# Performance work log

Hardware: AMD Instinct MI355X
Metric: run time of the kernel (lower is better)

The kernel has to match this reference:

```python
import jax, jax.numpy as jnp
import numpy as np

B, N, D, W, IMG = 16384, 20, 64, 64, 2048
NUM_USERS, NUM_ITEMS, NUM_INGRE = 100000, 201000, 33001


def setup_inputs() -> dict:
    key = jax.random.key(0)
    ks = jax.random.split(key, 24)
    s = lambda *sh: 1.0 / np.sqrt(sh[0])
    inp = {
        'user_input': jax.random.randint(ks[0], (B,), 0, NUM_USERS),
        'item_input': jax.random.randint(ks[1], (B,), 0, NUM_ITEMS),
        'ingre_input': jax.random.randint(ks[2], (B, N), 0, NUM_INGRE),
        'image_input': jax.random.normal(ks[3], (B, IMG), dtype=jnp.float32),
        'ingre_num': jax.random.randint(ks[4], (B,), 1, N + 1),
        'user_emb': jax.random.normal(ks[5], (NUM_USERS, D), dtype=jnp.float32) * 0.01,
        'item_emb': jax.random.normal(ks[6], (NUM_ITEMS, D), dtype=jnp.float32) * 0.01,
        'ingre_emb': jax.random.normal(ks[7], (NUM_INGRE, D), dtype=jnp.float32) * 0.01,
        'W_image_w': jax.random.normal(ks[8], (IMG, D), dtype=jnp.float32) * s(IMG),
        'W_image_b': jnp.zeros((D,), jnp.float32),
        'b_image': jnp.zeros((1, D), jnp.float32),
        'W_concat_w': jax.random.normal(ks[9], (3 * D, D), dtype=jnp.float32) * s(3 * D),
        'W_concat_b': jnp.zeros((D,), jnp.float32),
        'b_concat': jnp.zeros((1, D), jnp.float32),
        'h_w': jax.random.normal(ks[10], (D, 1), dtype=jnp.float32) * s(D),
        'h_b': jnp.zeros((1,), jnp.float32),
        'W_att_ingre_w': jax.random.normal(ks[11], (3 * D, W), dtype=jnp.float32) * s(3 * D),
        'W_att_ingre_b': jnp.zeros((W,), jnp.float32),
        'b_att_ingre': jnp.zeros((1, W), jnp.float32),
        'v': jnp.ones((W, 1), jnp.float32),
        'W_att_com_w': jax.random.normal(ks[12], (2 * D, W), dtype=jnp.float32) * s(2 * D),
        'W_att_com_b': jnp.zeros((W,), jnp.float32),
        'b_att_com': jnp.zeros((1, W), jnp.float32),
        'v_c': jnp.ones((W, 1), jnp.float32),
    }
    return inp


def reference(user_input, item_input, ingre_input, image_input, ingre_num,
              user_emb, item_emb, ingre_emb,
              W_image_w, W_image_b, b_image,
              W_concat_w, W_concat_b, b_concat, h_w, h_b,
              W_att_ingre_w, W_att_ingre_b, b_att_ingre, v,
              W_att_com_w, W_att_com_b, b_att_com, v_c):
    b = user_input.shape[0]
    ue = user_emb[user_input]                       # [B, D]
    ie = item_emb[item_input]                       # [B, D]
    qe = ingre_emb[ingre_input]                     # [B, N, D]
    img = image_input @ W_image_w + W_image_b + b_image  # [B, D]

    # ---- ingredient-level attention ----
    n = qe.shape[1]
    tile_p = jnp.broadcast_to(ue[:, None, :], (b, n, ue.shape[-1]))
    tile_i = jnp.broadcast_to(img[:, None, :], (b, n, img.shape[-1]))
    concat_v = jnp.concatenate([qe, tile_p, tile_i], axis=2)     # [B, N, 3D]
    mlp = jnp.tanh(concat_v @ W_att_ingre_w + W_att_ingre_b + b_att_ingre[0])  # [B, N, W]
    A_ = (mlp @ v)[..., 0]                                        # [B, N]
    mask = (jnp.arange(n)[None, :] < ingre_num[:, None]).astype(A_.dtype)
    A_ = A_ * mask + (1.0 - mask) * (-1e12)
    A = jax.nn.softmax(A_, axis=1)[..., None]                     # [B, N, 1]
    ingre_att = jnp.sum(A * qe, axis=1)                           # [B, D]

    # ---- component-level attention (faithful to original cat+view order) ----
    cp = jnp.concatenate([
        jnp.concatenate([ue, ie], axis=1),
        jnp.concatenate([ue, ingre_att], axis=1),
        jnp.concatenate([ue, img], axis=1),
    ], axis=0)                                                    # [3B, 2D]
    ch = jnp.tanh(cp @ W_att_com_w + W_att_com_b + b_att_com[0])  # [3B, W]
    scores = (ch @ v_c).reshape(b, -1)                            # [B, 3] (row-major, as torch .view)
    Bw = jax.nn.softmax(scores, axis=1)[..., None]                # [B, 3, 1]
    ce = jnp.stack([ie, ingre_att, img], axis=1)                  # [B, 3, D]
    item_att = jnp.sum(Bw * ce, axis=1)                           # [B, D]

    # ---- prediction head ----
    uic = jnp.concatenate([ue, item_att, ue * item_att], axis=-1) # [B, 3D]
    hidden = jax.nn.relu(uic @ W_concat_w + W_concat_b + b_concat[0])
    out = hidden @ h_w + h_b                                      # [B, 1]
    return out
```

## Files before the change

kernel.cpp:

```cpp
#include <hip/hip_runtime.h>
#include <hip/hip_fp16.h>

#define BB 16384
#define NN 20
#define DD 64
#define IMGK 2048

using bf16x8 = __attribute__((ext_vector_type(8))) short;
using f32x4  = __attribute__((ext_vector_type(4))) float;

__device__ __forceinline__ float waveReduceSum(float x) {
#pragma unroll
  for (int off = 32; off > 0; off >>= 1) x += __shfl_xor(x, off, 64);
  return x;
}

__device__ __forceinline__ float fast_tanh(float x) {
  float e = __expf(2.f * x);
  return 1.f - __fdividef(2.f, e + 1.f);
}

__device__ __forceinline__ short f2bf(float f) {
  union { float f; unsigned u; } c; c.f = f;
  unsigned r = c.u + 0x7fffu + ((c.u >> 16) & 1u);
  return (short)(r >> 16);
}
__device__ __forceinline__ float bf2f(short s) {
  union { unsigned u; float f; } c; c.u = ((unsigned)(unsigned short)s) << 16;
  return c.f;
}

__device__ __forceinline__ unsigned pack_hi(float a, float b) {
  unsigned ua = __float_as_uint(a), ub = __float_as_uint(b);
  return (ub & 0xffff0000u) | (ua >> 16);
}
__device__ __forceinline__ float trunc_bf(float a) {
  return __uint_as_float(__float_as_uint(a) & 0xffff0000u);
}

__global__ __launch_bounds__(256)
void prep_kernel(const float* __restrict__ Wimg, const float* __restrict__ W1,
                 short* __restrict__ Wf, short* __restrict__ W1f) {
  int i = blockIdx.x * 256 + threadIdx.x;
  if (i < 32768) {
    const int lane = i & 63;
    const int h = (i >> 6) & 1;
    const int tt = (i >> 7) & 3;
    const int ks = (i >> 9) & 3;
    const int kq = i >> 11;
    const int n = 16 * tt + (lane & 15);
    const int kb = kq * 128 + ks * 32 + (lane >> 4) * 8;
    union { short s[8]; bf16x8 v; } o;
#pragma unroll
    for (int j = 0; j < 8; ++j) {
      float f = Wimg[(size_t)(kb + j) * 64 + n];
      short hi = f2bf(f);
      o.s[j] = h == 0 ? hi : f2bf(f - bf2f(hi));
    }
    reinterpret_cast<bf16x8*>(Wf)[i] = o.v;
  } else if (i < 32768 + 1536) {
    const int j = i - 32768;
    const int lane = j & 63;
    const int wt = (j >> 6) & 3;
    const int ks = j >> 8;
    const int n = 16 * wt + (lane & 15);
    const int kb = ks * 32 + (lane >> 4) * 8;
    union { short s[8]; bf16x8 v; } o;
#pragma unroll
    for (int jj = 0; jj < 8; ++jj)
      o.s[jj] = f2bf(W1[(size_t)(kb + jj) * 64 + n]);
    reinterpret_cast<bf16x8*>(W1f)[j] = o.v;
  }
}

__global__ __launch_bounds__(256, 3)
void img_gemm_mfma(const float* __restrict__ img_in,
                   const short* __restrict__ Wf,
                   __half* __restrict__ pp) {
  __shared__ short wlds[16384];
  const int t = threadIdx.x;
  const int wave = t >> 6, lane = t & 63;
  const int lr = lane & 15, lk = lane >> 4;
  const int kq = blockIdx.x & 15, rg = blockIdx.x >> 4;
  __half* pout = pp + (size_t)kq * BB * 64;

  {
    const bf16x8* src = reinterpret_cast<const bf16x8*>(Wf + (size_t)kq * 16384);
    bf16x8* dst = reinterpret_cast<bf16x8*>(wlds);
    for (int i = t; i < 2048; i += 256) dst[i] = src[i];
  }
  __syncthreads();
  const bf16x8* wp = reinterpret_cast<const bf16x8*>(wlds);

#pragma unroll 1
  for (int c = 0; c < 4; ++c) {
    const int r0 = rg * 256 + wave * 64 + c * 16;
    const float* ar = img_in + (size_t)(r0 + lr) * IMGK + kq * 128 + lk * 8;
    float4 A[4][2];
#pragma unroll
    for (int ks = 0; ks < 4; ++ks) {
      A[ks][0] = *reinterpret_cast<const float4*>(ar + ks * 32);
      A[ks][1] = *reinterpret_cast<const float4*>(ar + ks * 32 + 4);
    }
    __builtin_amdgcn_sched_barrier(0);
    f32x4 aHH[4], aER[4];
#pragma unroll
    for (int tt = 0; tt < 4; ++tt) {
      aHH[tt] = (f32x4){0.f, 0.f, 0.f, 0.f};
      aER[tt] = (f32x4){0.f, 0.f, 0.f, 0.f};
    }
#pragma unroll
    for (int ks = 0; ks < 4; ++ks) {
      float4 va = A[ks][0], vb = A[ks][1];
      union { unsigned u[4]; bf16x8 v; } hi, lo;
      hi.u[0] = pack_hi(va.x, va.y);
      hi.u[1] = pack_hi(va.z, va.w);
      hi.u[2] = pack_hi(vb.x, vb.y);
      hi.u[3] = pack_hi(vb.z, vb.w);
      lo.u[0] = pack_hi(va.x - trunc_bf(va.x), va.y - trunc_bf(va.y));
      lo.u[1] = pack_hi(va.z - trunc_bf(va.z), va.w - trunc_bf(va.w));
      lo.u[2] = pack_hi(vb.x - trunc_bf(vb.x), vb.y - trunc_bf(vb.y));
      lo.u[3] = pack_hi(vb.z - trunc_bf(vb.z), vb.w - trunc_bf(vb.w));
#pragma unroll
      for (int tt = 0; tt < 4; ++tt) {
        bf16x8 wh = wp[((ks * 4 + tt) * 2 + 0) * 64 + lane];
        bf16x8 wl = wp[((ks * 4 + tt) * 2 + 1) * 64 + lane];
        aHH[tt] = __builtin_amdgcn_mfma_f32_16x16x32_bf16(hi.v, wh, aHH[tt], 0, 0, 0);
        aER[tt] = __builtin_amdgcn_mfma_f32_16x16x32_bf16(hi.v, wl, aER[tt], 0, 0, 0);
        aER[tt] = __builtin_amdgcn_mfma_f32_16x16x32_bf16(lo.v, wh, aER[tt], 0, 0, 0);
      }
    }
#pragma unroll
    for (int tt = 0; tt < 4; ++tt)
#pragma unroll
      for (int r = 0; r < 4; ++r)
        pout[(size_t)(r0 + 4 * lk + r) * 64 + 16 * tt + lr] =
            __float2half(aHH[tt][r] + aER[tt][r]);
  }
}

__global__ __launch_bounds__(256, 3)
void mid_kernel(const int* __restrict__ user_input,
                const int* __restrict__ ingre_input,
                const int* __restrict__ ingre_num,
                const float* __restrict__ user_emb,
                const float* __restrict__ ingre_emb,
                const __half* __restrict__ pp,
                const float* __restrict__ Wb, const float* __restrict__ bimg,
                const short* __restrict__ W1f,
                const float* __restrict__ Wib, const float* __restrict__ bai,
                const float* __restrict__ v,
                float* __restrict__ ws_img,
                float* __restrict__ ws_ia) {
  __shared__ short wflds[12288];
  __shared__ short qe_s[4][32][88];
  __shared__ short ui_s[4][128];
  __shared__ float sc_s[4][32];
  const int t = threadIdx.x;
  const int wave = t >> 6, lane = t & 63;
  const int lr = lane & 15, lk = lane >> 4;
  const int b = blockIdx.x * 4 + wave;

  for (int i = t; i < 1536; i += 256)
    reinterpret_cast<bf16x8*>(wflds)[i] = reinterpret_cast<const bf16x8*>(W1f)[i];

  float qv[NN];
#pragma unroll
  for (int n = 0; n < NN; ++n) {
    const int gi = ingre_input[b * NN + n];
    qv[n] = ingre_emb[(size_t)gi * 64 + lane];
  }
  float s = Wb[lane] + bimg[lane];
#pragma unroll
  for (int kq = 0; kq < 16; ++kq)
    s += __half2float(pp[(size_t)kq * BB * 64 + (size_t)b * 64 + lane]);
  const int u = user_input[b];
  const float ue = user_emb[(size_t)u * 64 + lane];
  ws_img[(size_t)b * 64 + lane] = s;
  float vv[4], biasw[4];
#pragma unroll
  for (int wt = 0; wt < 4; ++wt) {
    vv[wt] = v[16 * wt + lr];
    biasw[wt] = Wib[16 * wt + lr] + bai[16 * wt + lr];
  }

#pragma unroll
  for (int n = 0; n < NN; ++n) qe_s[wave][n][lane] = f2bf(qv[n]);
#pragma unroll
  for (int n = NN; n < 32; ++n) qe_s[wave][n][lane] = 0;
  ui_s[wave][lane] = f2bf(ue);
  ui_s[wave][64 + lane] = f2bf(s);
  __syncthreads();

  bf16x8 aq0[2], aq1[2], au[4];
#pragma unroll
  for (int ks = 0; ks < 2; ++ks) {
    aq0[ks] = *reinterpret_cast<const bf16x8*>(&qe_s[wave][lr][ks * 32 + lk * 8]);
    aq1[ks] = *reinterpret_cast<const bf16x8*>(&qe_s[wave][16 + lr][ks * 32 + lk * 8]);
  }
#pragma unroll
  for (int ks = 0; ks < 4; ++ks)
    au[ks] = *reinterpret_cast<const bf16x8*>(&ui_s[wave][ks * 32 + lk * 8]);

  const bf16x8* wp = reinterpret_cast<const bf16x8*>(wflds);
  f32x4 accq[2][4], accb[4];
#pragma unroll
  for (int wt = 0; wt < 4; ++wt) {
    accq[0][wt] = (f32x4){0.f, 0.f, 0.f, 0.f};
    accq[1][wt] = (f32x4){0.f, 0.f, 0.f, 0.f};
    accb[wt] = (f32x4){0.f, 0.f, 0.f, 0.f};
  }
#pragma unroll
  for (int ks = 0; ks < 2; ++ks)
#pragma unroll
    for (int wt = 0; wt < 4; ++wt) {
      bf16x8 w = wp[(ks * 4 + wt) * 64 + lane];
      accq[0][wt] = __builtin_amdgcn_mfma_f32_16x16x32_bf16(aq0[ks], w, accq[0][wt], 0, 0, 0);
      accq[1][wt] = __builtin_amdgcn_mfma_f32_16x16x32_bf16(aq1[ks], w, accq[1][wt], 0, 0, 0);
    }
#pragma unroll
  for (int ks = 2; ks < 6; ++ks)
#pragma unroll
    for (int wt = 0; wt < 4; ++wt) {
      bf16x8 w = wp[(ks * 4 + wt) * 64 + lane];
      accb[wt] = __builtin_amdgcn_mfma_f32_16x16x32_bf16(au[ks - 2], w, accb[wt], 0, 0, 0);
    }
  float basew[4];
#pragma unroll
  for (int wt = 0; wt < 4; ++wt) basew[wt] = accb[wt][0] + biasw[wt];

  float sp[2][4];
#pragma unroll
  for (int nt = 0; nt < 2; ++nt)
#pragma unroll
    for (int r = 0; r < 4; ++r) {
      float sv = 0.f;
#pragma unroll
      for (int wt = 0; wt < 4; ++wt) {
        float x = accq[nt][wt][r] + basew[wt];
        sv = fmaf(fast_tanh(x), vv[wt], sv);
      }
      sp[nt][r] = sv;
    }
#pragma unroll
  for (int off = 1; off < 16; off <<= 1)
#pragma unroll
    for (int nt = 0; nt < 2; ++nt)
#pragma unroll
      for (int r = 0; r < 4; ++r) sp[nt][r] += __shfl_xor(sp[nt][r], off, 64);
  if (lr == 0) {
#pragma unroll
    for (int r = 0; r < 4; ++r) {
      sc_s[wave][4 * lk + r] = sp[0][r];
      sc_s[wave][16 + 4 * lk + r] = sp[1][r];
    }
  }
  asm volatile("s_waitcnt lgkmcnt(0)" ::: "memory");
  float scn[NN];
#pragma unroll
  for (int q = 0; q < 5; ++q) {
    float4 s4 = *reinterpret_cast<const float4*>(&sc_s[wave][4 * q]);
    scn[4 * q + 0] = s4.x; scn[4 * q + 1] = s4.y;
    scn[4 * q + 2] = s4.z; scn[4 * q + 3] = s4.w;
  }
  asm volatile("s_waitcnt lgkmcnt(0)" ::: "memory");
  const int num = ingre_num[b];
  float m = -3e38f;
#pragma unroll
  for (int n = 0; n < NN; ++n) {
    scn[n] = (n < num) ? scn[n] : -1e12f;
    m = fmaxf(m, scn[n]);
  }
  float ssum = 0.f;
#pragma unroll
  for (int n = 0; n < NN; ++n) {
    scn[n] = __expf(scn[n] - m);
    ssum += scn[n];
  }
  const float inv = __fdividef(1.f, ssum);
  float ia = 0.f;
#pragma unroll
  for (int n = 0; n < NN; ++n) ia = fmaf(scn[n], qv[n], ia);
  ws_ia[(size_t)b * 64 + lane] = ia * inv;
}

__global__ __launch_bounds__(256, 4)
void com_score_kernel(const int* __restrict__ user_input,
                      const int* __restrict__ item_input,
                      const float* __restrict__ user_emb,
                      const float* __restrict__ item_emb,
                      const float* __restrict__ Wc,
                      const float* __restrict__ Wcb,
                      const float* __restrict__ bat,
                      const float* __restrict__ vc,
                      const float* __restrict__ ws_img,
                      const float* __restrict__ ws_ia,
                      float* __restrict__ ws_flat) {
  __shared__ float Wclds[128 * 64];
  __shared__ float x_s[4][4][64];
  const int t = threadIdx.x;
  for (int i = t; i < 128 * 64 / 4; i += 256)
    reinterpret_cast<float4*>(Wclds)[i] = reinterpret_cast<const float4*>(Wc)[i];
  __syncthreads();
  const int wave = t >> 6, lane = t & 63;
  const float bb = Wcb[lane] + bat[lane];
  const float vcl = vc[lane];
  const int b0 = blockIdx.x * 16 + wave * 4;
#pragma unroll 1
  for (int bi = 0; bi < 4; ++bi) {
    const int b = b0 + bi;
    const int u = user_input[b];
    const int it = item_input[b];
    x_s[wave][0][lane] = user_emb[(size_t)u * 64 + lane];
    x_s[wave][1][lane] = item_emb[(size_t)it * 64 + lane];
    x_s[wave][2][lane] = ws_ia[(size_t)b * 64 + lane];
    x_s[wave][3][lane] = ws_img[(size_t)b * 64 + lane];
    asm volatile("s_waitcnt lgkmcnt(0)" ::: "memory");
    const float4* u4 = reinterpret_cast<const float4*>(&x_s[wave][0][0]);
    float up = 0.f;
#pragma unroll
    for (int d0 = 0; d0 < 16; ++d0) {
      float4 q = u4[d0];
      int d = d0 * 4;
      up = fmaf(q.x, Wclds[(d + 0) * 64 + lane],
           fmaf(q.y, Wclds[(d + 1) * 64 + lane],
           fmaf(q.z, Wclds[(d + 2) * 64 + lane],
           fmaf(q.w, Wclds[(d + 3) * 64 + lane], up))));
    }
    float sc[3];
#pragma unroll
    for (int c = 0; c < 3; ++c) {
      const float4* y4 = reinterpret_cast<const float4*>(&x_s[wave][1 + c][0]);
      float s = bb + up;
#pragma unroll
      for (int d0 = 0; d0 < 16; ++d0) {
        float4 q = y4[d0];
        int d = 64 + d0 * 4;
        s = fmaf(q.x, Wclds[(d + 0) * 64 + lane],
            fmaf(q.y, Wclds[(d + 1) * 64 + lane],
            fmaf(q.z, Wclds[(d + 2) * 64 + lane],
            fmaf(q.w, Wclds[(d + 3) * 64 + lane], s))));
      }
      sc[c] = waveReduceSum(fast_tanh(s) * vcl);
    }
    if (lane == 0) {
      ws_flat[b] = sc[0];
      ws_flat[BB + b] = sc[1];
      ws_flat[2 * BB + b] = sc[2];
    }
    asm volatile("s_waitcnt lgkmcnt(0)" ::: "memory");
  }
}

__global__ __launch_bounds__(256, 3)
void head_kernel(const int* __restrict__ user_input,
                 const int* __restrict__ item_input,
                 const float* __restrict__ user_emb,
                 const float* __restrict__ item_emb,
                 const float* __restrict__ Wcat,
                 const float* __restrict__ Wcatb,
                 const float* __restrict__ bcat,
                 const float* __restrict__ hw,
                 const float* __restrict__ hb,
                 const float* __restrict__ ws_img,
                 const float* __restrict__ ws_ia,
                 const float* __restrict__ ws_flat,
                 float* __restrict__ out) {
  __shared__ float Wlds[192 * 64];
  __shared__ float ue_s[4][64];
  __shared__ float itt_s[4][64];
  const int t = threadIdx.x;
  for (int i = t; i < 192 * 64 / 4; i += 256)
    reinterpret_cast<float4*>(Wlds)[i] = reinterpret_cast<const float4*>(Wcat)[i];
  __syncthreads();
  const int wave = t >> 6, lane = t & 63;
  const float bb = Wcatb[lane] + bcat[lane];
  const float hwl = hw[lane];
  const float hbv = hb[0];
  const int b0 = blockIdx.x * 16 + wave * 4;
#pragma unroll 1
  for (int bi = 0; bi < 4; ++bi) {
    const int b = b0 + bi;
    const float s0 = ws_flat[3 * b + 0];
    const float s1 = ws_flat[3 * b + 1];
    const float s2 = ws_flat[3 * b + 2];
    const float m = fmaxf(s0, fmaxf(s1, s2));
    const float e0 = __expf(s0 - m), e1 = __expf(s1 - m), e2 = __expf(s2 - m);
    const float inv = 1.0f / (e0 + e1 + e2);
    const int u = user_input[b];
    const int it = item_input[b];
    const float uev = user_emb[(size_t)u * 64 + lane];
    const float itt = (e0 * item_emb[(size_t)it * 64 + lane] +
                       e1 * ws_ia[(size_t)b * 64 + lane] +
                       e2 * ws_img[(size_t)b * 64 + lane]) * inv;
    ue_s[wave][lane] = uev;
    itt_s[wave][lane] = itt;
    asm volatile("s_waitcnt lgkmcnt(0)" ::: "memory");
    const float4* u4 = reinterpret_cast<const float4*>(&ue_s[wave][0]);
    const float4* i4 = reinterpret_cast<const float4*>(&itt_s[wave][0]);
    float h = bb;
#pragma unroll
    for (int d0 = 0; d0 < 16; ++d0) {
      float4 uu = u4[d0];
      float4 ii = i4[d0];
      int d = d0 * 4;
      h = fmaf(uu.x, Wlds[(d + 0) * 64 + lane], h);
      h = fmaf(ii.x, Wlds[(64 + d + 0) * 64 + lane], h);
      h = fmaf(uu.x * ii.x, Wlds[(128 + d + 0) * 64 + lane], h);
      h = fmaf(uu.y, Wlds[(d + 1) * 64 + lane], h);
      h = fmaf(ii.y, Wlds[(64 + d + 1) * 64 + lane], h);
      h = fmaf(uu.y * ii.y, Wlds[(128 + d + 1) * 64 + lane], h);
      h = fmaf(uu.z, Wlds[(d + 2) * 64 + lane], h);
      h = fmaf(ii.z, Wlds[(64 + d + 2) * 64 + lane], h);
      h = fmaf(uu.z * ii.z, Wlds[(128 + d + 2) * 64 + lane], h);
      h = fmaf(uu.w, Wlds[(d + 3) * 64 + lane], h);
      h = fmaf(ii.w, Wlds[(64 + d + 3) * 64 + lane], h);
      h = fmaf(uu.w * ii.w, Wlds[(128 + d + 3) * 64 + lane], h);
    }
    h = fmaxf(h, 0.f) * hwl;
    float o = waveReduceSum(h);
    if (lane == 0) out[b] = o + hbv;
    asm volatile("s_waitcnt lgkmcnt(0)" ::: "memory");
  }
}

extern "C" void kernel_launch(void* const* d_in, const int* in_sizes, int n_in,
                              void* d_out, int out_size, void* d_ws, size_t ws_size,
                              hipStream_t stream) {
  (void)in_sizes; (void)n_in; (void)out_size; (void)ws_size;
  const int* user_input = (const int*)d_in[0];
  const int* item_input = (const int*)d_in[1];
  const int* ingre_input = (const int*)d_in[2];
  const float* image_input = (const float*)d_in[3];
  const int* ingre_num = (const int*)d_in[4];
  const float* user_emb = (const float*)d_in[5];
  const float* item_emb = (const float*)d_in[6];
  const float* ingre_emb = (const float*)d_in[7];
  const float* W_image_w = (const float*)d_in[8];
  const float* W_image_b = (const float*)d_in[9];
  const float* b_image = (const float*)d_in[10];
  const float* W_concat_w = (const float*)d_in[11];
  const float* W_concat_b = (const float*)d_in[12];
  const float* b_concat = (const float*)d_in[13];
  const float* h_w = (const float*)d_in[14];
  const float* h_b = (const float*)d_in[15];
  const float* W_att_ingre_w = (const float*)d_in[16];
  const float* W_att_ingre_b = (const float*)d_in[17];
  const float* b_att_ingre = (const float*)d_in[18];
  const float* v = (const float*)d_in[19];
  const float* W_att_com_w = (const float*)d_in[20];
  const float* W_att_com_b = (const float*)d_in[21];
  const float* b_att_com = (const float*)d_in[22];
  const float* v_c = (const float*)d_in[23];

  float* ws = (float*)d_ws;
  float* ws_img = ws;
  float* ws_ia = ws + (size_t)BB * 64;
  float* ws_flat = ws + (size_t)2 * BB * 64;
  short* Wf = (short*)(ws + (size_t)2 * BB * 64 + 3 * BB);
  short* W1f = Wf + (size_t)16 * 16384;
  __half* pp = (__half*)(W1f + 12288);
  float* out = (float*)d_out;

  prep_kernel<<<(32768 + 1536 + 255) / 256, 256, 0, stream>>>(
      W_image_w, W_att_ingre_w, Wf, W1f);
  img_gemm_mfma<<<1024, 256, 0, stream>>>(image_input, Wf, pp);
  mid_kernel<<<BB / 4, 256, 0, stream>>>(user_input, ingre_input, ingre_num,
                                         user_emb, ingre_emb, pp,
                                         W_image_b, b_image, W1f,
                                         W_att_ingre_b, b_att_ingre, v,
                                         ws_img, ws_ia);
  com_score_kernel<<<BB / 16, 256, 0, stream>>>(user_input, item_input, user_emb, item_emb,
                                                W_att_com_w, W_att_com_b, b_att_com, v_c,
                                                ws_img, ws_ia, ws_flat);
  head_kernel<<<BB / 16, 256, 0, stream>>>(user_input, item_input, user_emb, item_emb,
                                           W_concat_w, W_concat_b, b_concat, h_w, h_b,
                                           ws_img, ws_ia, ws_flat, out);
}
```

Measured before the change: 139.9 us.

## Split image GEMM K into 32 slices and stage tiles via direct global-to-LDS loads

The image projection GEMM now splits K into 32 slices of 64 instead of 16 slices of 128, and each block handles 64 rows instead of 256. Both the weight slice and an XOR-swizzled A tile are loaded with global_load_lds straight into shared memory, replacing per-thread register loads. Occupancy is raised to 5 blocks per CU and the grid grows to 8192 blocks. In exchange the fp16 partial-sum buffer doubles to 32 slices, so mid_kernel must read and reduce twice as many partials per row.

```diff
diff --git a/kernel.cpp b/kernel.cpp
--- a/kernel.cpp
+++ b/kernel.cpp
@@ -8,6 +8,12 @@
 
 using bf16x8 = __attribute__((ext_vector_type(8))) short;
 using f32x4  = __attribute__((ext_vector_type(4))) float;
+
+typedef __attribute__((address_space(1))) const unsigned int GUint;
+typedef __attribute__((address_space(3))) unsigned int LUint;
+__device__ __forceinline__ void gl_lds16(const void* g, void* l) {
+  __builtin_amdgcn_global_load_lds((GUint*)g, (LUint*)l, 16, 0, 0);
+}
 
 __device__ __forceinline__ float waveReduceSum(float x) {
 #pragma unroll
@@ -46,10 +52,10 @@
     const int lane = i & 63;
     const int h = (i >> 6) & 1;
     const int tt = (i >> 7) & 3;
-    const int ks = (i >> 9) & 3;
-    const int kq = i >> 11;
+    const int ks = (i >> 9) & 1;
+    const int kq = i >> 10;
     const int n = 16 * tt + (lane & 15);
-    const int kb = kq * 128 + ks * 32 + (lane >> 4) * 8;
+    const int kb = kq * 64 + ks * 32 + (lane >> 4) * 8;
     union { short s[8]; bf16x8 v; } o;
 #pragma unroll
     for (int j = 0; j < 8; ++j) {
@@ -73,70 +79,78 @@
   }
 }
 
-__global__ __launch_bounds__(256, 3)
+__global__ __launch_bounds__(256, 5)
 void img_gemm_mfma(const float* __restrict__ img_in,
                    const short* __restrict__ Wf,
                    __half* __restrict__ pp) {
-  __shared__ short wlds[16384];
+  __shared__ short wlds[8192];
+  __shared__ float alds[4096];
   const int t = threadIdx.x;
   const int wave = t >> 6, lane = t & 63;
   const int lr = lane & 15, lk = lane >> 4;
-  const int kq = blockIdx.x & 15, rg = blockIdx.x >> 4;
+  const int kq = blockIdx.x & 31, rgb = blockIdx.x >> 5;
+  const int r0 = rgb * 64;
   __half* pout = pp + (size_t)kq * BB * 64;
 
-  {
-    const bf16x8* src = reinterpret_cast<const bf16x8*>(Wf + (size_t)kq * 16384);
-    bf16x8* dst = reinterpret_cast<bf16x8*>(wlds);
-    for (int i = t; i < 2048; i += 256) dst[i] = src[i];
-  }
+  const short* wsrc = Wf + (size_t)kq * 8192;
+#pragma unroll
+  for (int i = 0; i < 4; ++i) {
+    int j = i * 256 + t;
+    gl_lds16(wsrc + j * 8, wlds + j * 8);
+  }
+#pragma unroll
+  for (int i = 0; i < 4; ++i) {
+    int j = i * 256 + t;
+    int r = j >> 4, c = j & 15;
+    int gc = (c ^ (r & 7)) * 4;
+    gl_lds16(img_in + (size_t)(r0 + r) * IMGK + kq * 64 + gc, alds + j * 4);
+  }
+  asm volatile("s_waitcnt vmcnt(0)" ::: "memory");
   __syncthreads();
+
+  const int arow = wave * 16 + lr;
+  const int rx = arow & 7;
+  float4 Af[2][2];
+#pragma unroll
+  for (int ks = 0; ks < 2; ++ks) {
+    const int s0 = ks * 8 + lk * 2;
+    Af[ks][0] = *reinterpret_cast<const float4*>(alds + arow * 64 + (s0 ^ rx) * 4);
+    Af[ks][1] = *reinterpret_cast<const float4*>(alds + arow * 64 + ((s0 + 1) ^ rx) * 4);
+  }
   const bf16x8* wp = reinterpret_cast<const bf16x8*>(wlds);
-
-#pragma unroll 1
-  for (int c = 0; c < 4; ++c) {
-    const int r0 = rg * 256 + wave * 64 + c * 16;
-    const float* ar = img_in + (size_t)(r0 + lr) * IMGK + kq * 128 + lk * 8;
-    float4 A[4][2];
-#pragma unroll
-    for (int ks = 0; ks < 4; ++ks) {
-      A[ks][0] = *reinterpret_cast<const float4*>(ar + ks * 32);
-      A[ks][1] = *reinterpret_cast<const float4*>(ar + ks * 32 + 4);
-    }
-    __builtin_amdgcn_sched_barrier(0);
-    f32x4 aHH[4], aER[4];
+  f32x4 aHH[4], aER[4];
+#pragma unroll
+  for (int tt = 0; tt < 4; ++tt) {
+    aHH[tt] = (f32x4){0.f, 0.f, 0.f, 0.f};
+    aER[tt] = (f32x4){0.f, 0.f, 0.f, 0.f};
+  }
+#pragma unroll
+  for (int ks = 0; ks < 2; ++ks) {
+    float4 va = Af[ks][0], vb = Af[ks][1];
+    union { unsigned u[4]; bf16x8 v; } hi, lo;
+    hi.u[0] = pack_hi(va.x, va.y);
+    hi.u[1] = pack_hi(va.z, va.w);
+    hi.u[2] = pack_hi(vb.x, vb.y);
+    hi.u[3] = pack_hi(vb.z, vb.w);
+    lo.u[0] = pack_hi(va.x - trunc_bf(va.x), va.y - trunc_bf(va.y));
+    lo.u[1] = pack_hi(va.z - trunc_bf(va.z), va.w - trunc_bf(va.w));
+    lo.u[2] = pack_hi(vb.x - trunc_bf(vb.x), vb.y - trunc_bf(vb.y));
+    lo.u[3] = pack_hi(vb.z - trunc_bf(vb.z), vb.w - trunc_bf(vb.w));
 #pragma unroll
     for (int tt = 0; tt < 4; ++tt) {
-      aHH[tt] = (f32x4){0.f, 0.f, 0.f, 0.f};
-      aER[tt] = (f32x4){0.f, 0.f, 0.f, 0.f};
-    }
-#pragma unroll
-    for (int ks = 0; ks < 4; ++ks) {
-      float4 va = A[ks][0], vb = A[ks][1];
-      union { unsigned u[4]; bf16x8 v; } hi, lo;
-      hi.u[0] = pack_hi(va.x, va.y);
-      hi.u[1] = pack_hi(va.z, va.w);
-      hi.u[2] = pack_hi(vb.x, vb.y);
-      hi.u[3] = pack_hi(vb.z, vb.w);
-      lo.u[0] = pack_hi(va.x - trunc_bf(va.x), va.y - trunc_bf(va.y));
-      lo.u[1] = pack_hi(va.z - trunc_bf(va.z), va.w - trunc_bf(va.w));
-      lo.u[2] = pack_hi(vb.x - trunc_bf(vb.x), vb.y - trunc_bf(vb.y));
-      lo.u[3] = pack_hi(vb.z - trunc_bf(vb.z), vb.w - trunc_bf(vb.w));
-#pragma unroll
-      for (int tt = 0; tt < 4; ++tt) {
-        bf16x8 wh = wp[((ks * 4 + tt) * 2 + 0) * 64 + lane];
-        bf16x8 wl = wp[((ks * 4 + tt) * 2 + 1) * 64 + lane];
-        aHH[tt] = __builtin_amdgcn_mfma_f32_16x16x32_bf16(hi.v, wh, aHH[tt], 0, 0, 0);
-        aER[tt] = __builtin_amdgcn_mfma_f32_16x16x32_bf16(hi.v, wl, aER[tt], 0, 0, 0);
-        aER[tt] = __builtin_amdgcn_mfma_f32_16x16x32_bf16(lo.v, wh, aER[tt], 0, 0, 0);
-      }
-    }
-#pragma unroll
-    for (int tt = 0; tt < 4; ++tt)
-#pragma unroll
-      for (int r = 0; r < 4; ++r)
-        pout[(size_t)(r0 + 4 * lk + r) * 64 + 16 * tt + lr] =
-            __float2half(aHH[tt][r] + aER[tt][r]);
-  }
+      bf16x8 wh = wp[((ks * 4 + tt) * 2 + 0) * 64 + lane];
+      bf16x8 wl = wp[((ks * 4 + tt) * 2 + 1) * 64 + lane];
+      aHH[tt] = __builtin_amdgcn_mfma_f32_16x16x32_bf16(hi.v, wh, aHH[tt], 0, 0, 0);
+      aER[tt] = __builtin_amdgcn_mfma_f32_16x16x32_bf16(hi.v, wl, aER[tt], 0, 0, 0);
+      aER[tt] = __builtin_amdgcn_mfma_f32_16x16x32_bf16(lo.v, wh, aER[tt], 0, 0, 0);
+    }
+  }
+#pragma unroll
+  for (int tt = 0; tt < 4; ++tt)
+#pragma unroll
+    for (int r = 0; r < 4; ++r)
+      pout[(size_t)(r0 + wave * 16 + 4 * lk + r) * 64 + 16 * tt + lr] =
+          __float2half(aHH[tt][r] + aER[tt][r]);
 }
 
 __global__ __launch_bounds__(256, 3)
@@ -172,7 +186,7 @@
   }
   float s = Wb[lane] + bimg[lane];
 #pragma unroll
-  for (int kq = 0; kq < 16; ++kq)
+  for (int kq = 0; kq < 32; ++kq)
     s += __half2float(pp[(size_t)kq * BB * 64 + (size_t)b * 64 + lane]);
   const int u = user_input[b];
   const float ue = user_emb[(size_t)u * 64 + lane];
@@ -458,13 +472,13 @@
   float* ws_ia = ws + (size_t)BB * 64;
   float* ws_flat = ws + (size_t)2 * BB * 64;
   short* Wf = (short*)(ws + (size_t)2 * BB * 64 + 3 * BB);
-  short* W1f = Wf + (size_t)16 * 16384;
+  short* W1f = Wf + (size_t)32 * 8192;
   __half* pp = (__half*)(W1f + 12288);
   float* out = (float*)d_out;
 
   prep_kernel<<<(32768 + 1536 + 255) / 256, 256, 0, stream>>>(
       W_image_w, W_att_ingre_w, Wf, W1f);
-  img_gemm_mfma<<<1024, 256, 0, stream>>>(image_input, Wf, pp);
+  img_gemm_mfma<<<8192, 256, 0, stream>>>(image_input, Wf, pp);
   mid_kernel<<<BB / 4, 256, 0, stream>>>(user_input, ingre_input, ingre_num,
                                          user_emb, ingre_emb, pp,
                                          W_image_b, b_image, W1f,
```

Result: slower. 144.6 us (+3.3%).
